# Performance work log

Hardware: AMD Instinct MI355X
Metric: run time of the kernel (lower is better)

The kernel has to match this reference:

```python
import jax, jax.numpy as jnp
import numpy as np

N_ATOMS = 200_000   # total atoms across the batch of structures
D_IN = 256          # input feature dim
D_OUT = 256         # per-species expert output dim
N_SPECIES = 4       # number of atomic species (experts)
N_STRUCT = 2_000    # number of structures (segments for index_add)


def setup_inputs() -> dict:
    key = jax.random.key(0)
    k0, k1, k2, k3, k4 = jax.random.split(key, 5)
    x = jax.random.normal(k0, (N_ATOMS, D_IN), dtype=jnp.float32)
    # per-species expert weights (the 'models' ModuleDict -> Linear per specie)
    W = jax.random.normal(k1, (N_SPECIES, D_IN, D_OUT), dtype=jnp.float32) * (1.0 / np.float32(np.sqrt(D_IN)))
    b = jax.random.normal(k2, (N_SPECIES, D_OUT), dtype=jnp.float32) * 0.01
    central_species = jax.random.randint(k3, (N_ATOMS,), 0, N_SPECIES, dtype=jnp.int32)
    structural_indices = jnp.sort(jax.random.randint(k4, (N_ATOMS,), 0, N_STRUCT, dtype=jnp.int32))
    return {"x": x, "W": W, "b": b,
            "central_species": central_species,
            "structural_indices": structural_indices}


def reference(x, W, b, central_species, structural_indices):
    # CentralSplitter -> per-species expert (Linear) -> CentralUniter,
    # expressed as masked dense compute (same math per atom as gather/scatter):
    # each atom's row goes through exactly the expert of its species.
    n_species = W.shape[0]
    out = jnp.zeros((x.shape[0], W.shape[2]), dtype=x.dtype)
    for s in range(n_species):  # small fixed expert loop
        mask = (central_species == s)[:, None]
        out = out + jnp.where(mask, x @ W[s] + b[s], jnp.zeros((), x.dtype))
    # Accumulator: index_add over structural_indices == segment sum per structure
    return jax.ops.segment_sum(out, structural_indices, num_segments=N_STRUCT)
```

## Files before the change

### kernel.cpp

```cpp
#include <hip/hip_runtime.h>
#include <hip/hip_bf16.h>

#define N_ATOMS   200000
#define D_IN      256
#define D_OUT     256
#define N_SPECIES 4
#define N_STRUCT  2000
#define M_PAD     2048
#define KFLAT     1024
#define SEG_D     8
#define SEG_AHEAD 7
#define WT_BLOCKS 512

typedef __attribute__((ext_vector_type(8))) short bf16x8;
typedef __attribute__((ext_vector_type(4))) float f32x4;

typedef const __attribute__((address_space(1))) float gfloat;
typedef __attribute__((address_space(3))) float lfloat;

__device__ inline unsigned short f2bf(float f) {
    unsigned int u = __float_as_uint(f);
    unsigned int r = (u + 0x7fffu + ((u >> 16) & 1u)) >> 16;
    return (unsigned short)r;
}


__device__ __forceinline__ int lb64(const int* __restrict__ sidx, int key, int lane) {
    int lo = 0, hi = N_ATOMS;
    while (hi - lo > 64) {
        int step = (hi - lo + 63) >> 6;
        int pos  = lo + lane * step;
        int v    = (pos < hi) ? sidx[pos] : 0x7fffffff;
        unsigned long long m = __ballot(v < key);
        int c = __popcll(m);
        int nlo = (c == 0)  ? lo : (lo + (c - 1) * step + 1);
        int nhi = (c == 64) ? hi : min(hi, lo + c * step);
        lo = nlo; hi = nhi;
    }
    int pos = lo + lane;
    int v   = (pos < hi) ? sidx[pos] : 0x7fffffff;
    unsigned long long m = __ballot(v < key);
    return lo + __popcll(m);
}

__global__ __launch_bounds__(256) void k_fused(
        const float* __restrict__ x, const float* __restrict__ W,
        const int* __restrict__ spec, const int* __restrict__ sidx,
        unsigned short* __restrict__ Wt, unsigned short* __restrict__ S,
        float* __restrict__ cnt) {

    __shared__ __align__(16) float ring[4][SEG_D][256];

    int t = threadIdx.x;
    int bid = blockIdx.x;

    if (bid < WT_BLOCKS) {
        int gid = bid * 256 + t;
        int o   = gid * 4;
        int kbg = o >> 14;
        int nn  = (o >> 6) & 255;
        int kp  = o & 63;
        int s   = kbg >> 2, kb = kbg & 3;
        int k0  = kb * 64 + kp;
        const float* wb = W + (size_t)s * 65536 + (size_t)k0 * 256 + nn;
        ushort4 u;
        u.x = f2bf(wb[0]);
        u.y = f2bf(wb[256]);
        u.z = f2bf(wb[512]);
        u.w = f2bf(wb[768]);
        *(ushort4*)(Wt + o) = u;
        return;
    }

    int w = t >> 6, lane = t & 63;
    int g = (bid - WT_BLOCKS) * 4 + w;
    if (g >= N_STRUCT) return;

    int s0 = lb64(sidx, g,     lane);
    int s1 = lb64(sidx, g + 1, lane);
    int n  = s1 - s0;

    f32x4 a0 = (f32x4){0.f,0.f,0.f,0.f}, a1 = a0, a2 = a0, a3 = a0;
    float c0 = 0.f, c1 = 0.f, c2 = 0.f, c3 = 0.f;

    if (n > 0) {
        int nm1 = n - 1;
        const float* gp0 = x + (size_t)s0 * 256 + lane * 4;

        unsigned long long m0[4], m1[4];
        bool fits = (n <= 256);
        if (fits) {
#pragma unroll
            for (int c = 0; c < 4; ++c) {
                int sv = spec[s0 + min(c * 64 + lane, nm1)];
                m0[c] = __ballot((sv & 1) != 0);
                m1[c] = __ballot((sv & 2) != 0);
            }
        }

        asm volatile("s_waitcnt vmcnt(0)" ::: "memory");

#pragma unroll
        for (int j = 0; j < SEG_AHEAD; ++j) {
            int rr = min(j, nm1);
            __builtin_amdgcn_global_load_lds(
                (gfloat*)(gp0 + (size_t)rr * 256),
                (lfloat*)&ring[w][j][0], 16, 0, 0);
        }

#define CONS4(vv, sp)                                                     \
        switch (sp) {                                                     \
            case 0: a0 += vv; c0 += 1.f; break;                           \
            case 1: a1 += vv; c1 += 1.f; break;                           \
            case 2: a2 += vv; c2 += 1.f; break;                           \
            default: a3 += vv; c3 += 1.f; break; }

        if (fits) {
#pragma unroll
            for (int c = 0; c < 4; ++c) {
                int cb = c * 64;
                if (cb < n) {
                    unsigned long long mm0 = m0[c], mm1 = m1[c];
                    int ce = min(n, cb + 64);
                    for (int j = cb; j < ce; ++j) {
                        asm volatile("s_waitcnt vmcnt(6)" ::: "memory");
                        f32x4 v = *(const f32x4*)&ring[w][j & (SEG_D - 1)][lane * 4];
                        int r  = j - cb;
                        int sp = (int)((mm0 >> r) & 1ull) | ((int)((mm1 >> r) & 1ull) << 1);
                        CONS4(v, sp);
                        int rr = min(j + SEG_AHEAD, nm1);
                        __builtin_amdgcn_global_load_lds(
                            (gfloat*)(gp0 + (size_t)rr * 256),
                            (lfloat*)&ring[w][(j + SEG_AHEAD) & (SEG_D - 1)][0], 16, 0, 0);
                    }
                }
            }
        } else {
            for (int cb = 0; cb < n; cb += 64) {
                int spv = spec[s0 + min(cb + lane, nm1)];
                asm volatile("s_waitcnt vmcnt(0)" ::: "memory");
                unsigned long long mm0 = __ballot((spv & 1) != 0);
                unsigned long long mm1 = __ballot((spv & 2) != 0);
                int ce = min(n, cb + 64);
                for (int j = cb; j < ce; ++j) {
                    f32x4 v = *(const f32x4*)&ring[w][j & (SEG_D - 1)][lane * 4];
                    int r  = j - cb;
                    int sp = (int)((mm0 >> r) & 1ull) | ((int)((mm1 >> r) & 1ull) << 1);
                    CONS4(v, sp);
                    int rr = min(j + SEG_AHEAD, nm1);
                    __builtin_amdgcn_global_load_lds(
                        (gfloat*)(gp0 + (size_t)rr * 256),
                        (lfloat*)&ring[w][(j + SEG_AHEAD) & (SEG_D - 1)][0], 16, 0, 0);
                    asm volatile("s_waitcnt vmcnt(6)" ::: "memory");
                }
            }
        }
#undef CONS4
    }

    unsigned short* Sg = S + (size_t)g * KFLAT + lane * 4;
    ushort4 u;
    u.x = f2bf(a0[0]); u.y = f2bf(a0[1]); u.z = f2bf(a0[2]); u.w = f2bf(a0[3]);
    *(ushort4*)(Sg + 0)   = u;
    u.x = f2bf(a1[0]); u.y = f2bf(a1[1]); u.z = f2bf(a1[2]); u.w = f2bf(a1[3]);
    *(ushort4*)(Sg + 256) = u;
    u.x = f2bf(a2[0]); u.y = f2bf(a2[1]); u.z = f2bf(a2[2]); u.w = f2bf(a2[3]);
    *(ushort4*)(Sg + 512) = u;
    u.x = f2bf(a3[0]); u.y = f2bf(a3[1]); u.z = f2bf(a3[2]); u.w = f2bf(a3[3]);
    *(ushort4*)(Sg + 768) = u;

    if (lane == 0) {
        float4 c4; c4.x = c0; c4.y = c1; c4.z = c2; c4.w = c3;
        *(float4*)(cnt + (size_t)g * 4) = c4;
    }
}

__global__ __launch_bounds__(256) void k_gemm5(
        const unsigned short* __restrict__ S, const float* __restrict__ cnt,
        const float* __restrict__ b, const unsigned short* __restrict__ Wt,
        float* __restrict__ out) {

    __shared__ __align__(16) f32x4 red[4][2][2][64];

    int t = threadIdx.x, w = t >> 6, lane = t & 63;
    int l15 = lane & 15, l4 = lane >> 4;
    int bid = blockIdx.x;
    int g0 = (bid >> 3) * 32;
    int c0 = (bid & 7) * 32;

    f32x4 acc[2][2];
#pragma unroll
    for (int m = 0; m < 2; ++m)
#pragma unroll
        for (int n = 0; n < 2; ++n) acc[m][n] = (f32x4){0.f, 0.f, 0.f, 0.f};

    const unsigned short* arow = S + (size_t)(g0 + l15) * KFLAT + w * 256 + l4 * 8;
    const unsigned short* wsp  = Wt + (size_t)w * 4 * 16384 + l4 * 8;

#pragma unroll
    for (int kb = 0; kb < 4; ++kb) {
#pragma unroll
        for (int ks = 0; ks < 2; ++ks) {
            bf16x8 af[2];
#pragma unroll
            for (int m = 0; m < 2; ++m)
                af[m] = *(const bf16x8*)(arow + (size_t)m * 16 * KFLAT + kb * 64 + ks * 32);
#pragma unroll
            for (int n = 0; n < 2; ++n) {
                bf16x8 bfr = *(const bf16x8*)(wsp + (size_t)kb * 16384
                                + (size_t)(c0 + n * 16 + l15) * 64 + ks * 32);
#pragma unroll
                for (int m = 0; m < 2; ++m)
                    acc[m][n] = __builtin_amdgcn_mfma_f32_16x16x32_bf16(af[m], bfr, acc[m][n], 0, 0, 0);
            }
        }
    }

#pragma unroll
    for (int m = 0; m < 2; ++m)
#pragma unroll
        for (int n = 0; n < 2; ++n) red[w][m][n][lane] = acc[m][n];
    __syncthreads();

    {
        int mw = w >> 1, nw = w & 1;
        f32x4 sum = red[0][mw][nw][lane] + red[1][mw][nw][lane]
                  + red[2][mw][nw][lane] + red[3][mw][nw][lane];

        int col = c0 + nw * 16 + l15;
        float bv[4];
#pragma unroll
        for (int s = 0; s < 4; ++s) bv[s] = b[s * 256 + col];

#pragma unroll
        for (int r = 0; r < 4; ++r) {
            int grow = g0 + mw * 16 + l4 * 4 + r;
            if (grow < N_STRUCT) {
                float4 c4 = *(const float4*)(cnt + (size_t)grow * 4);
                out[(size_t)grow * 256 + col] =
                    sum[r] + c4.x * bv[0] + c4.y * bv[1]
                           + c4.z * bv[2] + c4.w * bv[3];
            }
        }
    }
}

extern "C" void kernel_launch(void* const* d_in, const int* in_sizes, int n_in,
                              void* d_out, int out_size, void* d_ws, size_t ws_size,
                              hipStream_t stream) {
    const float* x    = (const float*)d_in[0];
    const float* W    = (const float*)d_in[1];
    const float* b    = (const float*)d_in[2];
    const int* spec   = (const int*)d_in[3];
    const int* sidx   = (const int*)d_in[4];
    float* out        = (float*)d_out;

    char* ws = (char*)d_ws;
    unsigned short* Wt = (unsigned short*)ws;
    unsigned short* S  = (unsigned short*)(ws + 524288);
    float* cnt  = (float*)(ws + 4718592);

    k_fused<<<WT_BLOCKS + (N_STRUCT + 3) / 4, 256, 0, stream>>>(x, W, spec, sidx, Wt, S, cnt);
    k_gemm5<<<(M_PAD / 32) * (D_OUT / 32), 256, 0, stream>>>(S, cnt, b, Wt, out);
}
```

Before: 50.60 us.

## Assign one block per structure with each wave owning a quarter of the features

The segment-sum phase used to give each wave a whole structure, with every lane handling 4 features through 16-byte LDS-direct loads. Now each block handles one structure and each of its 4 waves covers 64 columns, one float per lane, using 4-byte global-to-LDS loads. The intent is four times more parallelism across CUs (2000 blocks instead of 500) and less per-wave serial work on long segments. In exchange the loads and stores become narrower, every wave repeats the binary search and species ballots, and there are more blocks to schedule.

Result: slower. 57.75 us (+14.1%).

```diff
diff --git a/kernel.cpp b/kernel.cpp
--- a/kernel.cpp
+++ b/kernel.cpp
@@ -49,7 +49,7 @@
         unsigned short* __restrict__ Wt, unsigned short* __restrict__ S,
         float* __restrict__ cnt) {
 
-    __shared__ __align__(16) float ring[4][SEG_D][256];
+    __shared__ __align__(16) float ring[SEG_D][256];
 
     int t = threadIdx.x;
     int bid = blockIdx.x;
@@ -73,19 +73,19 @@
     }
 
     int w = t >> 6, lane = t & 63;
-    int g = (bid - WT_BLOCKS) * 4 + w;
-    if (g >= N_STRUCT) return;
+    int g = bid - WT_BLOCKS;
 
     int s0 = lb64(sidx, g,     lane);
     int s1 = lb64(sidx, g + 1, lane);
     int n  = s1 - s0;
 
-    f32x4 a0 = (f32x4){0.f,0.f,0.f,0.f}, a1 = a0, a2 = a0, a3 = a0;
+    float a0 = 0.f, a1 = 0.f, a2 = 0.f, a3 = 0.f;
     float c0 = 0.f, c1 = 0.f, c2 = 0.f, c3 = 0.f;
 
     if (n > 0) {
         int nm1 = n - 1;
-        const float* gp0 = x + (size_t)s0 * 256 + lane * 4;
+        const float* gp0 = x + (size_t)s0 * 256 + w * 64 + lane;
+        lfloat* ldst = (lfloat*)&ring[0][w * 64];
 
         unsigned long long m0[4], m1[4];
         bool fits = (n <= 256);
@@ -105,10 +105,10 @@
             int rr = min(j, nm1);
             __builtin_amdgcn_global_load_lds(
                 (gfloat*)(gp0 + (size_t)rr * 256),
-                (lfloat*)&ring[w][j][0], 16, 0, 0);
-        }
-
-#define CONS4(vv, sp)                                                     \
+                (lfloat*)&ring[j][w * 64], 4, 0, 0);
+        }
+
+#define CONS1(vv, sp)                                                     \
         switch (sp) {                                                     \
             case 0: a0 += vv; c0 += 1.f; break;                           \
             case 1: a1 += vv; c1 += 1.f; break;                           \
@@ -124,14 +124,14 @@
                     int ce = min(n, cb + 64);
                     for (int j = cb; j < ce; ++j) {
                         asm volatile("s_waitcnt vmcnt(6)" ::: "memory");
-                        f32x4 v = *(const f32x4*)&ring[w][j & (SEG_D - 1)][lane * 4];
+                        float v = ring[j & (SEG_D - 1)][w * 64 + lane];
                         int r  = j - cb;
                         int sp = (int)((mm0 >> r) & 1ull) | ((int)((mm1 >> r) & 1ull) << 1);
-                        CONS4(v, sp);
+                        CONS1(v, sp);
                         int rr = min(j + SEG_AHEAD, nm1);
                         __builtin_amdgcn_global_load_lds(
                             (gfloat*)(gp0 + (size_t)rr * 256),
-                            (lfloat*)&ring[w][(j + SEG_AHEAD) & (SEG_D - 1)][0], 16, 0, 0);
+                            (lfloat*)&ring[(j + SEG_AHEAD) & (SEG_D - 1)][w * 64], 4, 0, 0);
                     }
                 }
             }
@@ -143,33 +143,29 @@
                 unsigned long long mm1 = __ballot((spv & 2) != 0);
                 int ce = min(n, cb + 64);
                 for (int j = cb; j < ce; ++j) {
-                    f32x4 v = *(const f32x4*)&ring[w][j & (SEG_D - 1)][lane * 4];
+                    float v = ring[j & (SEG_D - 1)][w * 64 + lane];
                     int r  = j - cb;
                     int sp = (int)((mm0 >> r) & 1ull) | ((int)((mm1 >> r) & 1ull) << 1);
-                    CONS4(v, sp);
+                    CONS1(v, sp);
                     int rr = min(j + SEG_AHEAD, nm1);
                     __builtin_amdgcn_global_load_lds(
                         (gfloat*)(gp0 + (size_t)rr * 256),
-                        (lfloat*)&ring[w][(j + SEG_AHEAD) & (SEG_D - 1)][0], 16, 0, 0);
+                        (lfloat*)&ring[(j + SEG_AHEAD) & (SEG_D - 1)][w * 64], 4, 0, 0);
                     asm volatile("s_waitcnt vmcnt(6)" ::: "memory");
                 }
             }
         }
-#undef CONS4
-    }
-
-    unsigned short* Sg = S + (size_t)g * KFLAT + lane * 4;
-    ushort4 u;
-    u.x = f2bf(a0[0]); u.y = f2bf(a0[1]); u.z = f2bf(a0[2]); u.w = f2bf(a0[3]);
-    *(ushort4*)(Sg + 0)   = u;
-    u.x = f2bf(a1[0]); u.y = f2bf(a1[1]); u.z = f2bf(a1[2]); u.w = f2bf(a1[3]);
-    *(ushort4*)(Sg + 256) = u;
-    u.x = f2bf(a2[0]); u.y = f2bf(a2[1]); u.z = f2bf(a2[2]); u.w = f2bf(a2[3]);
-    *(ushort4*)(Sg + 512) = u;
-    u.x = f2bf(a3[0]); u.y = f2bf(a3[1]); u.z = f2bf(a3[2]); u.w = f2bf(a3[3]);
-    *(ushort4*)(Sg + 768) = u;
-
-    if (lane == 0) {
+#undef CONS1
+        (void)ldst;
+    }
+
+    unsigned short* Sg = S + (size_t)g * KFLAT + w * 64 + lane;
+    Sg[0]   = f2bf(a0);
+    Sg[256] = f2bf(a1);
+    Sg[512] = f2bf(a2);
+    Sg[768] = f2bf(a3);
+
+    if (w == 0 && lane == 0) {
         float4 c4; c4.x = c0; c4.y = c1; c4.z = c2; c4.w = c3;
         *(float4*)(cnt + (size_t)g * 4) = c4;
     }
@@ -260,6 +256,6 @@
     unsigned short* S  = (unsigned short*)(ws + 524288);
     float* cnt  = (float*)(ws + 4718592);
 
-    k_fused<<<WT_BLOCKS + (N_STRUCT + 3) / 4, 256, 0, stream>>>(x, W, spec, sidx, Wt, S, cnt);
+    k_fused<<<WT_BLOCKS + N_STRUCT, 256, 0, stream>>>(x, W, spec, sidx, Wt, S, cnt);
     k_gemm5<<<(M_PAD / 32) * (D_OUT / 32), 256, 0, stream>>>(S, cnt, b, Wt, out);
 }
```

## Split each structure's segment sum across two wavefronts with LDS reduction

Applied to the files above, without the earlier changes.

Each structure's atom range is now split in half and processed by two waves of the block. The partial per-species sums and counts are then combined through shared memory before the bf16 store. The goal is to double the number of waves streaming x, giving more memory-level parallelism and shorter per-wave serial chains. The cost is a block-wide sync, extra LDS traffic, and twice as many segment blocks to launch.

Result: slower. 70.36 us (+39.0%).

```diff
diff --git a/kernel.cpp b/kernel.cpp
--- a/kernel.cpp
+++ b/kernel.cpp
@@ -50,6 +50,8 @@
         float* __restrict__ cnt) {
 
     __shared__ __align__(16) float ring[4][SEG_D][256];
+    __shared__ __align__(16) f32x4 red[2][4][64];
+    __shared__ float csl[2][4];
 
     int t = threadIdx.x;
     int bid = blockIdx.x;
@@ -73,26 +75,30 @@
     }
 
     int w = t >> 6, lane = t & 63;
-    int g = (bid - WT_BLOCKS) * 4 + w;
-    if (g >= N_STRUCT) return;
+    int gi   = w >> 1;
+    int half = w & 1;
+    int g = (bid - WT_BLOCKS) * 2 + gi;
 
     int s0 = lb64(sidx, g,     lane);
     int s1 = lb64(sidx, g + 1, lane);
     int n  = s1 - s0;
+    int nh = (n + 1) >> 1;
+    int hs = s0 + half * nh;
+    int hn = half ? (n - nh) : nh;
 
     f32x4 a0 = (f32x4){0.f,0.f,0.f,0.f}, a1 = a0, a2 = a0, a3 = a0;
     float c0 = 0.f, c1 = 0.f, c2 = 0.f, c3 = 0.f;
 
-    if (n > 0) {
-        int nm1 = n - 1;
-        const float* gp0 = x + (size_t)s0 * 256 + lane * 4;
+    if (hn > 0) {
+        int nm1 = hn - 1;
+        const float* gp0 = x + (size_t)hs * 256 + lane * 4;
 
         unsigned long long m0[4], m1[4];
-        bool fits = (n <= 256);
+        bool fits = (hn <= 256);
         if (fits) {
 #pragma unroll
             for (int c = 0; c < 4; ++c) {
-                int sv = spec[s0 + min(c * 64 + lane, nm1)];
+                int sv = spec[hs + min(c * 64 + lane, nm1)];
                 m0[c] = __ballot((sv & 1) != 0);
                 m1[c] = __ballot((sv & 2) != 0);
             }
@@ -119,9 +125,9 @@
 #pragma unroll
             for (int c = 0; c < 4; ++c) {
                 int cb = c * 64;
-                if (cb < n) {
+                if (cb < hn) {
                     unsigned long long mm0 = m0[c], mm1 = m1[c];
-                    int ce = min(n, cb + 64);
+                    int ce = min(hn, cb + 64);
                     for (int j = cb; j < ce; ++j) {
                         asm volatile("s_waitcnt vmcnt(6)" ::: "memory");
                         f32x4 v = *(const f32x4*)&ring[w][j & (SEG_D - 1)][lane * 4];
@@ -136,12 +142,12 @@
                 }
             }
         } else {
-            for (int cb = 0; cb < n; cb += 64) {
-                int spv = spec[s0 + min(cb + lane, nm1)];
+            for (int cb = 0; cb < hn; cb += 64) {
+                int spv = spec[hs + min(cb + lane, nm1)];
                 asm volatile("s_waitcnt vmcnt(0)" ::: "memory");
                 unsigned long long mm0 = __ballot((spv & 1) != 0);
                 unsigned long long mm1 = __ballot((spv & 2) != 0);
-                int ce = min(n, cb + 64);
+                int ce = min(hn, cb + 64);
                 for (int j = cb; j < ce; ++j) {
                     f32x4 v = *(const f32x4*)&ring[w][j & (SEG_D - 1)][lane * 4];
                     int r  = j - cb;
@@ -158,20 +164,41 @@
 #undef CONS4
     }
 
-    unsigned short* Sg = S + (size_t)g * KFLAT + lane * 4;
-    ushort4 u;
-    u.x = f2bf(a0[0]); u.y = f2bf(a0[1]); u.z = f2bf(a0[2]); u.w = f2bf(a0[3]);
-    *(ushort4*)(Sg + 0)   = u;
-    u.x = f2bf(a1[0]); u.y = f2bf(a1[1]); u.z = f2bf(a1[2]); u.w = f2bf(a1[3]);
-    *(ushort4*)(Sg + 256) = u;
-    u.x = f2bf(a2[0]); u.y = f2bf(a2[1]); u.z = f2bf(a2[2]); u.w = f2bf(a2[3]);
-    *(ushort4*)(Sg + 512) = u;
-    u.x = f2bf(a3[0]); u.y = f2bf(a3[1]); u.z = f2bf(a3[2]); u.w = f2bf(a3[3]);
-    *(ushort4*)(Sg + 768) = u;
-
-    if (lane == 0) {
-        float4 c4; c4.x = c0; c4.y = c1; c4.z = c2; c4.w = c3;
-        *(float4*)(cnt + (size_t)g * 4) = c4;
+    if (half == 1) {
+        red[gi][0][lane] = a0;
+        red[gi][1][lane] = a1;
+        red[gi][2][lane] = a2;
+        red[gi][3][lane] = a3;
+        if (lane == 0) {
+            csl[gi][0] = c0; csl[gi][1] = c1; csl[gi][2] = c2; csl[gi][3] = c3;
+        }
+    }
+    __syncthreads();
+    if (half == 0) {
+        a0 += red[gi][0][lane];
+        a1 += red[gi][1][lane];
+        a2 += red[gi][2][lane];
+        a3 += red[gi][3][lane];
+
+        unsigned short* Sg = S + (size_t)g * KFLAT + lane * 4;
+        ushort4 u;
+        u.x = f2bf(a0[0]); u.y = f2bf(a0[1]); u.z = f2bf(a0[2]); u.w = f2bf(a0[3]);
+        *(ushort4*)(Sg + 0)   = u;
+        u.x = f2bf(a1[0]); u.y = f2bf(a1[1]); u.z = f2bf(a1[2]); u.w = f2bf(a1[3]);
+        *(ushort4*)(Sg + 256) = u;
+        u.x = f2bf(a2[0]); u.y = f2bf(a2[1]); u.z = f2bf(a2[2]); u.w = f2bf(a2[3]);
+        *(ushort4*)(Sg + 512) = u;
+        u.x = f2bf(a3[0]); u.y = f2bf(a3[1]); u.z = f2bf(a3[2]); u.w = f2bf(a3[3]);
+        *(ushort4*)(Sg + 768) = u;
+
+        if (lane == 0) {
+            float4 c4;
+            c4.x = c0 + csl[gi][0];
+            c4.y = c1 + csl[gi][1];
+            c4.z = c2 + csl[gi][2];
+            c4.w = c3 + csl[gi][3];
+            *(float4*)(cnt + (size_t)g * 4) = c4;
+        }
     }
 }
 
@@ -260,6 +287,6 @@
     unsigned short* S  = (unsigned short*)(ws + 524288);
     float* cnt  = (float*)(ws + 4718592);
 
-    k_fused<<<WT_BLOCKS + (N_STRUCT + 3) / 4, 256, 0, stream>>>(x, W, spec, sidx, Wt, S, cnt);
+    k_fused<<<WT_BLOCKS + (N_STRUCT + 1) / 2, 256, 0, stream>>>(x, W, spec, sidx, Wt, S, cnt);
     k_gemm5<<<(M_PAD / 32) * (D_OUT / 32), 256, 0, stream>>>(S, cnt, b, Wt, out);
 }
```
